# Kernel optimization log

Hardware: AMD Instinct MI355X
Metric: run time of the kernel (lower is better)

The kernel has to match this reference:

```python
import jax, jax.numpy as jnp
import numpy as np

N = 50000      # nodes per graph batch (per side)
E = 600000     # edges per side
B = 4096       # number of graphs (drug pairs)
D = 128        # node_dim == hidden_dim
K = 128        # kge_dim
R = 86         # rel_total
L = 3          # n_iter
EPS = 1e-5


def setup_inputs() -> dict:
    key = jax.random.key(0)
    ks = jax.random.split(key, 16)
    inp = {}
    inp["x1"] = jax.random.normal(ks[0], (N, D), jnp.float32)
    inp["x2"] = jax.random.normal(ks[1], (N, D), jnp.float32)
    inp["edge_index1"] = jax.random.randint(ks[2], (2, E), 0, N)
    inp["edge_index2"] = jax.random.randint(ks[3], (2, E), 0, N)
    inp["batch1"] = jnp.sort(jax.random.randint(ks[4], (N,), 0, B))
    inp["batch2"] = jnp.sort(jax.random.randint(ks[5], (N,), 0, B))
    inp["rel"] = jax.random.randint(ks[6], (B,), 0, R)
    # SAGEConv params, stacked over L layers (all [D,D] since node_dim==hidden_dim)
    sc = 0.05
    inp["Wl"] = jax.random.normal(ks[7], (L, D, D), jnp.float32) * sc   # lin on aggregated neighbors (has bias)
    inp["bl"] = jnp.zeros((L, D), jnp.float32)
    inp["Wr"] = jax.random.normal(ks[8], (L, D, D), jnp.float32) * sc   # root (self) lin, no bias
    # BatchNorm (eval mode: running stats)
    inp["bn_gamma"] = jnp.ones((L, D), jnp.float32)
    inp["bn_beta"] = jnp.zeros((L, D), jnp.float32)
    inp["bn_mean"] = jnp.zeros((L, D), jnp.float32)
    inp["bn_var"] = jnp.ones((L, D), jnp.float32)
    # relation embedding + final MLP
    inp["kge"] = jax.random.normal(ks[9], (R, K), jnp.float32)
    inp["W1"] = jax.random.normal(ks[10], (2 * D + K, D), jnp.float32) * sc
    inp["b1"] = jnp.zeros((D,), jnp.float32)
    inp["W2"] = jax.random.normal(ks[11], (D, 1), jnp.float32) * sc
    inp["b2"] = jnp.zeros((1,), jnp.float32)
    return inp


def _gnn(x, edge_index, Wl, bl, Wr, g, b, m, v):
    src, dst = edge_index[0], edge_index[1]
    deg = jax.ops.segment_sum(jnp.ones((E,), x.dtype), dst, num_segments=N)
    deg = jnp.maximum(deg, 1.0)[:, None]
    for i in range(L):
        agg = jax.ops.segment_sum(x[src], dst, num_segments=N) / deg  # mean aggregation
        h = agg @ Wl[i] + bl[i] + x @ Wr[i]                           # SAGEConv
        h = (h - m[i]) * (g[i] / jnp.sqrt(v[i] + EPS)) + b[i]         # BN (eval)
        x = jax.nn.relu(h)                                            # dropout = identity (eval)
    return x


def reference(x1, edge_index1, batch1, x2, edge_index2, batch2, rel,
              Wl, bl, Wr, bn_gamma, bn_beta, bn_mean, bn_var,
              kge, W1, b1, W2, b2):
    h1 = _gnn(x1, edge_index1, Wl, bl, Wr, bn_gamma, bn_beta, bn_mean, bn_var)
    h2 = _gnn(x2, edge_index2, Wl, bl, Wr, bn_gamma, bn_beta, bn_mean, bn_var)
    p1 = jax.ops.segment_sum(h1, batch1, num_segments=B)  # global_add_pool
    p2 = jax.ops.segment_sum(h2, batch2, num_segments=B)
    r = kge[rel]                                          # [B, K]
    z = jnp.concatenate([p1, p2, r], axis=-1)             # [B, 2D+K]
    h = jax.nn.relu(z @ W1 + b1)
    out = h @ W2 + b2
    return out.reshape(-1)
```

## Files before the change

kernel.cpp:

```cpp
#include <hip/hip_runtime.h>

#define NN 50000
#define NE 600000
#define NB 4096
#define DD 128
#define EPSV 1e-5f
#define NBKT 196
#define NCHUNK 256
#define CHSZ ((NE + NCHUNK - 1) / NCHUNK)

typedef __bf16 bf16x8 __attribute__((ext_vector_type(8)));
typedef float f32x4 __attribute__((ext_vector_type(4)));

__device__ inline unsigned short f2bf(float f) {
    unsigned u = __float_as_uint(f);
    u = (u + 0x7FFFu + ((u >> 16) & 1u)) >> 16;
    return (unsigned short)u;
}
__device__ inline float bf2f(unsigned short h) {
    return __uint_as_float(((unsigned)h) << 16);
}

__global__ void k_cvt(const float* __restrict__ x1, const float* __restrict__ x2,
                      unsigned short* __restrict__ xh, unsigned short* __restrict__ xl) {
    int i = blockIdx.x * 256 + threadIdx.x;
    if (i >= 2 * NN * 32) return;
    const float* x = (i < NN * 32) ? x1 : x2;
    int j = (i < NN * 32) ? i : i - NN * 32;
    float4 v = ((const float4*)x)[j];
    ushort4 h, l;
    h.x = f2bf(v.x); l.x = f2bf(v.x - bf2f(h.x));
    h.y = f2bf(v.y); l.y = f2bf(v.y - bf2f(h.y));
    h.z = f2bf(v.z); l.z = f2bf(v.z - bf2f(h.z));
    h.w = f2bf(v.w); l.w = f2bf(v.w - bf2f(h.w));
    ((ushort4*)xh)[i] = h;
    ((ushort4*)xl)[i] = l;
}

__global__ void k_wcvt(const float* __restrict__ W1, unsigned* __restrict__ wtp) {
    int t = blockIdx.x * 256 + threadIdx.x;
    if (t >= 128 * 384) return;
    int n = t / 384;
    int k = t - n * 384;
    float w = W1[k * 128 + n];
    unsigned short h = f2bf(w);
    unsigned short l = f2bf(w - bf2f(h));
    wtp[t] = ((unsigned)h << 16) | (unsigned)l;
}

__global__ void k_wfrag(const float* __restrict__ Wl, const float* __restrict__ Wr,
                        unsigned short* __restrict__ wf) {
    int t = blockIdx.x * 256 + threadIdx.x;
    if (t >= 3 * 128 * 256) return;
    int k = t & 255;
    int n = (t >> 8) & 127;
    int l = t >> 15;
    float w = (k < 128) ? Wl[l * 16384 + k * 128 + n] : Wr[l * 16384 + (k - 128) * 128 + n];
    unsigned short h = f2bf(w);
    unsigned short lo = f2bf(w - bf2f(h));
    int ntile = n >> 4, fm = n & 15, kc = k >> 5, kq = (k & 31) >> 3, j = k & 7;
    size_t pos = (size_t)l * 65536 + (size_t)(ntile * 8 + kc) * 1024 + (size_t)(kq * 16 + fm) * 8 + j;
    wf[pos] = h;
    wf[pos + 512] = lo;
}

__global__ void k_hist(const int* __restrict__ d0, const int* __restrict__ d1,
                       int* __restrict__ bcnt) {
    int side = (blockIdx.x >= NCHUNK) ? 1 : 0;
    int c = blockIdx.x - side * NCHUNK;
    const int* dst = side ? d1 : d0;
    int tid = threadIdx.x;
    __shared__ int h[NBKT];
    for (int i = tid; i < NBKT; i += 256) h[i] = 0;
    __syncthreads();
    int e0 = c * CHSZ, e1 = min(e0 + CHSZ, NE);
    for (int e = e0 + tid; e < e1; e += 256) atomicAdd(&h[dst[e] >> 8], 1);
    __syncthreads();
    int* bc = bcnt + ((size_t)side * NCHUNK + c) * NBKT;
    for (int i = tid; i < NBKT; i += 256) bc[i] = h[i];
}

__global__ void k_s1(int* __restrict__ bcnt, int* __restrict__ btot) {
    int side = (blockIdx.x >= NBKT) ? 1 : 0;
    int b = blockIdx.x - side * NBKT;
    int tid = threadIdx.x;
    int idx = ((size_t)side * NCHUNK + tid) * NBKT + b;
    int v = bcnt[idx];
    int lane = tid & 63, wv = tid >> 6;
    int x = v;
#pragma unroll
    for (int off = 1; off < 64; off <<= 1) {
        int y = __shfl_up(x, off, 64);
        if (lane >= off) x += y;
    }
    __shared__ int ws4[4];
    if (lane == 63) ws4[wv] = x;
    __syncthreads();
    int add = 0;
#pragma unroll
    for (int w = 0; w < 4; w++)
        if (w < wv) add += ws4[w];
    int incl = x + add;
    bcnt[idx] = incl - v;
    if (tid == 255) btot[side * NBKT + b] = incl;
}

__global__ void k_s2(const int* __restrict__ btot, int* __restrict__ bbase,
                     int* __restrict__ ptrC) {
    int side = blockIdx.x;
    int tid = threadIdx.x;
    int v = (tid < NBKT) ? btot[side * NBKT + tid] : 0;
    int lane = tid & 63, wv = tid >> 6;
    int x = v;
#pragma unroll
    for (int off = 1; off < 64; off <<= 1) {
        int y = __shfl_up(x, off, 64);
        if (lane >= off) x += y;
    }
    __shared__ int ws4[4];
    if (lane == 63) ws4[wv] = x;
    __syncthreads();
    int add = 0;
#pragma unroll
    for (int w = 0; w < 4; w++)
        if (w < wv) add += ws4[w];
    int incl = x + add;
    if (tid < NBKT) bbase[side * NBKT + tid] = incl - v;
    if (tid == 0 && side == 1) ptrC[2 * NN] = 2 * NE;
}

__global__ void k_part(const int* __restrict__ s0, const int* __restrict__ d0,
                       const int* __restrict__ s1, const int* __restrict__ d1,
                       const int* __restrict__ bcnt, const int* __restrict__ bbase,
                       int* __restrict__ part) {
    int side = (blockIdx.x >= NCHUNK) ? 1 : 0;
    int c = blockIdx.x - side * NCHUNK;
    const int* src = side ? s1 : s0;
    const int* dst = side ? d1 : d0;
    int tid = threadIdx.x;
    __shared__ int off[NBKT];
    const int* bc = bcnt + ((size_t)side * NCHUNK + c) * NBKT;
    for (int i = tid; i < NBKT; i += 256) off[i] = bbase[side * NBKT + i] + bc[i];
    __syncthreads();
    int e0 = c * CHSZ, e1 = min(e0 + CHSZ, NE);
    int* P = part + (size_t)side * NE;
    int soff = side * NN;
    for (int e = e0 + tid; e < e1; e += 256) {
        int d = dst[e];
        int pos = atomicAdd(&off[d >> 8], 1);
        P[pos] = ((src[e] + soff) << 8) | (d & 255);
    }
}

__global__ void k_csr(const int* __restrict__ part, const int* __restrict__ bbase,
                      int* __restrict__ ptrC, float* __restrict__ invdC,
                      int* __restrict__ csrC) {
    int side = (blockIdx.x >= NBKT) ? 1 : 0;
    int b = blockIdx.x - side * NBKT;
    int tid = threadIdx.x;
    const int* P = part + (size_t)side * NE;
    int base = bbase[side * NBKT + b];
    int endp = (b == NBKT - 1) ? NE : bbase[side * NBKT + b + 1];
    __shared__ int cnt[256];
    cnt[tid] = 0;
    __syncthreads();
    for (int e = base + tid; e < endp; e += 256) atomicAdd(&cnt[P[e] & 255], 1);
    __syncthreads();
    int v = cnt[tid];
    int lane = tid & 63, wv = tid >> 6;
    int x = v;
#pragma unroll
    for (int off = 1; off < 64; off <<= 1) {
        int y = __shfl_up(x, off, 64);
        if (lane >= off) x += y;
    }
    __shared__ int ws4[4];
    if (lane == 63) ws4[wv] = x;
    __syncthreads();
    int add = 0;
#pragma unroll
    for (int w = 0; w < 4; w++)
        if (w < wv) add += ws4[w];
    int excl = x + add - v;
    int node = (b << 8) + tid;
    if (node < NN) {
        ptrC[side * NN + node] = side * NE + base + excl;
        invdC[side * NN + node] = 1.0f / (float)(v > 1 ? v : 1);
    }
    __syncthreads();
    cnt[tid] = excl;
    __syncthreads();
    for (int e = base + tid; e < endp; e += 256) {
        int p = P[e];
        int pos = atomicAdd(&cnt[p & 255], 1);
        csrC[(size_t)side * NE + base + pos] = p >> 8;
    }
}

__global__ void k_gather(const unsigned short* __restrict__ xh, const int* __restrict__ ptr,
                         const int* __restrict__ csr, const float* __restrict__ invd,
                         unsigned short* __restrict__ aggH) {
    int wid = threadIdx.x >> 6;
    int lane = threadIdx.x & 63;
    int q = lane >> 4;
    int c = lane & 15;
    int n = blockIdx.x * 4 + wid;
    if (n >= 2 * NN) return;
    int beg = ptr[n], end = ptr[n + 1];
    float id = invd[n];
    float a[8];
#pragma unroll
    for (int k = 0; k < 8; k++) a[k] = 0.f;

    for (int base = beg; base < end; base += 64) {
        int cnt = min(end - base, 64);
        int idxv = csr[base + min(lane, cnt - 1)];
        for (int e0 = 0; e0 < cnt; e0 += 8) {
            int eA = e0 + q;
            int eB = e0 + 4 + q;
            int iA = __shfl(idxv, eA, 64);
            int iB = __shfl(idxv, eB, 64);
            float wA = (eA < cnt) ? 1.f : 0.f;
            float wB = (eB < cnt) ? 1.f : 0.f;
            uint4 vA = *(const uint4*)(xh + (((unsigned)iA << 7) + (c << 3)));
            uint4 vB = *(const uint4*)(xh + (((unsigned)iB << 7) + (c << 3)));
            a[0] += wA * __uint_as_float(vA.x << 16);
            a[1] += wA * __uint_as_float(vA.x & 0xffff0000u);
            a[2] += wA * __uint_as_float(vA.y << 16);
            a[3] += wA * __uint_as_float(vA.y & 0xffff0000u);
            a[4] += wA * __uint_as_float(vA.z << 16);
            a[5] += wA * __uint_as_float(vA.z & 0xffff0000u);
            a[6] += wA * __uint_as_float(vA.w << 16);
            a[7] += wA * __uint_as_float(vA.w & 0xffff0000u);
            a[0] += wB * __uint_as_float(vB.x << 16);
            a[1] += wB * __uint_as_float(vB.x & 0xffff0000u);
            a[2] += wB * __uint_as_float(vB.y << 16);
            a[3] += wB * __uint_as_float(vB.y & 0xffff0000u);
            a[4] += wB * __uint_as_float(vB.z << 16);
            a[5] += wB * __uint_as_float(vB.z & 0xffff0000u);
            a[6] += wB * __uint_as_float(vB.w << 16);
            a[7] += wB * __uint_as_float(vB.w & 0xffff0000u);
        }
    }
#pragma unroll
    for (int k = 0; k < 8; k++) {
        a[k] += __shfl_xor(a[k], 16, 64);
        a[k] += __shfl_xor(a[k], 32, 64);
    }
    if (q == 0) {
        unsigned short h0 = f2bf(a[0] * id), h1 = f2bf(a[1] * id);
        unsigned short h2 = f2bf(a[2] * id), h3 = f2bf(a[3] * id);
        unsigned short h4 = f2bf(a[4] * id), h5 = f2bf(a[5] * id);
        unsigned short h6 = f2bf(a[6] * id), h7 = f2bf(a[7] * id);
        uint4 o;
        o.x = (unsigned)h0 | ((unsigned)h1 << 16);
        o.y = (unsigned)h2 | ((unsigned)h3 << 16);
        o.z = (unsigned)h4 | ((unsigned)h5 << 16);
        o.w = (unsigned)h6 | ((unsigned)h7 << 16);
        *(uint4*)(aggH + (size_t)n * DD + c * 8) = o;
    }
}

__launch_bounds__(256)
__global__ void k_gemm2(const unsigned short* __restrict__ AH,
                        const unsigned short* __restrict__ XH, const unsigned short* __restrict__ XL,
                        const unsigned short* __restrict__ wf,
                        const float* __restrict__ bl, const float* __restrict__ g,
                        const float* __restrict__ be, const float* __restrict__ mn,
                        const float* __restrict__ vr,
                        unsigned short* __restrict__ OH, unsigned short* __restrict__ OL,
                        float* __restrict__ Of, int f32out) {
    int tid = threadIdx.x;
    int lane = tid & 63, w = tid >> 6;
    int fm = lane & 15, kq = lane >> 4;
    int m0 = blockIdx.x * 32;

    size_t rb0 = (size_t)(m0 + fm) * DD + kq * 8;
    size_t rb1 = rb0 + (size_t)16 * DD;
    const unsigned short* pA0 = AH + rb0;
    const unsigned short* pA1 = AH + rb1;
    const unsigned short* pXH0 = XH + rb0;
    const unsigned short* pXH1 = XH + rb1;
    const unsigned short* pXL0 = XL + rb0;
    const unsigned short* pXL1 = XL + rb1;
    const unsigned short* pW0 = wf + (size_t)(w * 2 + 0) * 8192 + lane * 8;
    const unsigned short* pW1 = wf + (size_t)(w * 2 + 1) * 8192 + lane * 8;

    f32x4 acc[2][2];
#pragma unroll
    for (int i = 0; i < 2; i++)
#pragma unroll
        for (int j = 0; j < 2; j++) acc[i][j] = (f32x4){0.f, 0.f, 0.f, 0.f};

#pragma unroll
    for (int c = 0; c < 8; c++) {
        bf16x8 a0h, a1h, a0l, a1l;
        if (c < 4) {
            a0h = *(const bf16x8*)(pA0 + c * 32);
            a1h = *(const bf16x8*)(pA1 + c * 32);
        } else {
            a0h = *(const bf16x8*)(pXH0 + (c - 4) * 32);
            a1h = *(const bf16x8*)(pXH1 + (c - 4) * 32);
            a0l = *(const bf16x8*)(pXL0 + (c - 4) * 32);
            a1l = *(const bf16x8*)(pXL1 + (c - 4) * 32);
        }
        bf16x8 w0h = *(const bf16x8*)(pW0 + c * 1024);
        bf16x8 w0l = *(const bf16x8*)(pW0 + c * 1024 + 512);
        bf16x8 w1h = *(const bf16x8*)(pW1 + c * 1024);
        bf16x8 w1l = *(const bf16x8*)(pW1 + c * 1024 + 512);
        acc[0][0] = __builtin_amdgcn_mfma_f32_16x16x32_bf16(a0h, w0h, acc[0][0], 0, 0, 0);
        acc[0][0] = __builtin_amdgcn_mfma_f32_16x16x32_bf16(a0h, w0l, acc[0][0], 0, 0, 0);
        acc[0][1] = __builtin_amdgcn_mfma_f32_16x16x32_bf16(a0h, w1h, acc[0][1], 0, 0, 0);
        acc[0][1] = __builtin_amdgcn_mfma_f32_16x16x32_bf16(a0h, w1l, acc[0][1], 0, 0, 0);
        acc[1][0] = __builtin_amdgcn_mfma_f32_16x16x32_bf16(a1h, w0h, acc[1][0], 0, 0, 0);
        acc[1][0] = __builtin_amdgcn_mfma_f32_16x16x32_bf16(a1h, w0l, acc[1][0], 0, 0, 0);
        acc[1][1] = __builtin_amdgcn_mfma_f32_16x16x32_bf16(a1h, w1h, acc[1][1], 0, 0, 0);
        acc[1][1] = __builtin_amdgcn_mfma_f32_16x16x32_bf16(a1h, w1l, acc[1][1], 0, 0, 0);
        if (c >= 4) {
            acc[0][0] = __builtin_amdgcn_mfma_f32_16x16x32_bf16(a0l, w0h, acc[0][0], 0, 0, 0);
            acc[0][1] = __builtin_amdgcn_mfma_f32_16x16x32_bf16(a0l, w1h, acc[0][1], 0, 0, 0);
            acc[1][0] = __builtin_amdgcn_mfma_f32_16x16x32_bf16(a1l, w0h, acc[1][0], 0, 0, 0);
            acc[1][1] = __builtin_amdgcn_mfma_f32_16x16x32_bf16(a1l, w1h, acc[1][1], 0, 0, 0);
        }
    }

    float scv[2], shv[2];
#pragma unroll
    for (int nt = 0; nt < 2; nt++) {
        int jj = w * 32 + nt * 16 + fm;
        float s = g[jj] * rsqrtf(vr[jj] + EPSV);
        scv[nt] = s;
        shv[nt] = (bl[jj] - mn[jj]) * s + be[jj];
    }
#pragma unroll
    for (int mt = 0; mt < 2; mt++) {
#pragma unroll
        for (int r = 0; r < 4; r++) {
            int grow = m0 + mt * 16 + kq * 4 + r;
#pragma unroll
            for (int nt = 0; nt < 2; nt++) {
                int gcol = w * 32 + nt * 16 + fm;
                float o = fmaxf(acc[mt][nt][r] * scv[nt] + shv[nt], 0.f);
                if (f32out) {
                    Of[(size_t)grow * DD + gcol] = o;
                } else {
                    unsigned short h = f2bf(o);
                    OH[(size_t)grow * DD + gcol] = h;
                    OL[(size_t)grow * DD + gcol] = f2bf(o - bf2f(h));
                }
            }
        }
    }
}

__launch_bounds__(128)
__global__ void k_pool2(const float* __restrict__ cf, const int* __restrict__ bt1,
                        const int* __restrict__ bt2, float* __restrict__ ppool) {
    int side = (blockIdx.x >= NB) ? 1 : 0;
    int b = blockIdx.x - side * NB;
    const int* batch = side ? bt2 : bt1;
    const float* h = cf + (size_t)side * NN * DD;
    __shared__ int sr[2];
    if (threadIdx.x < 2) {
        int target = b + (int)threadIdx.x;
        int lo = 0, hi = NN;
        while (lo < hi) {
            int mid = (lo + hi) >> 1;
            if (batch[mid] < target) lo = mid + 1; else hi = mid;
        }
        sr[threadIdx.x] = lo;
    }
    __syncthreads();
    int beg = sr[0], end = sr[1];
    int t = threadIdx.x;
    float acc = 0.f;
    for (int r = beg; r < end; r++) acc += h[(size_t)r * DD + t];
    ppool[((size_t)side * NB + b) * DD + t] = acc;
}

__global__ void k_zb(const float* __restrict__ ppool, const int* __restrict__ rel,
                     const float* __restrict__ kge,
                     unsigned short* __restrict__ zh, unsigned short* __restrict__ zl) {
    int t = blockIdx.x * 256 + threadIdx.x;
    if (t >= NB * 384) return;
    int b = t / 384;
    int j = t - b * 384;
    float v;
    if (j < 128) v = ppool[(size_t)b * DD + j];
    else if (j < 256) v = ppool[(size_t)NB * DD + (size_t)b * DD + (j - 128)];
    else v = kge[(size_t)rel[b] * 128 + (j - 256)];
    unsigned short h = f2bf(v);
    zh[t] = h;
    zl[t] = f2bf(v - bf2f(h));
}

__launch_bounds__(256)
__global__ void k_mlp2(const unsigned short* __restrict__ zh, const unsigned short* __restrict__ zl,
                       const unsigned* __restrict__ w1p,
                       const float* __restrict__ b1, const float* __restrict__ W2,
                       const float* __restrict__ b2, float* __restrict__ out) {
    __shared__ __align__(16) unsigned short sZ[2][32 * 40];
    __shared__ __align__(16) unsigned short sW[2][128 * 40];
    __shared__ float hpart[32][4];
    int tid = threadIdx.x;
    int m0 = blockIdx.x * 32;
    int lane = tid & 63, w = tid >> 6;
    int fm = lane & 15, q = lane >> 4;
    int wn = w * 32;

    f32x4 acc[2][2];
#pragma unroll
    for (int i = 0; i < 2; i++)
#pragma unroll
        for (int j = 0; j < 2; j++) acc[i][j] = (f32x4){0.f, 0.f, 0.f, 0.f};

    for (int c = 0; c < 12; c++) {
        int k0 = c * 32;
        __syncthreads();
        {
            int row = tid >> 3, seg = tid & 7;
            size_t off = (size_t)(m0 + row) * 384 + k0 + seg * 4;
            *(ushort4*)&sZ[0][row * 40 + seg * 4] = *(const ushort4*)(zh + off);
            *(ushort4*)&sZ[1][row * 40 + seg * 4] = *(const ushort4*)(zl + off);
        }
#pragma unroll
        for (int i = 0; i < 4; i++) {
            int u = tid + 256 * i;
            int row = u >> 3, seg = u & 7;
            uint4 val = *(const uint4*)(w1p + (size_t)row * 384 + k0 + seg * 4);
            ushort4 hi, lo;
            hi.x = val.x >> 16; hi.y = val.y >> 16; hi.z = val.z >> 16; hi.w = val.w >> 16;
            lo.x = val.x & 0xFFFF; lo.y = val.y & 0xFFFF; lo.z = val.z & 0xFFFF; lo.w = val.w & 0xFFFF;
            *(ushort4*)&sW[0][row * 40 + seg * 4] = hi;
            *(ushort4*)&sW[1][row * 40 + seg * 4] = lo;
        }
        __syncthreads();
        bf16x8 zfh[2], zfl[2];
#pragma unroll
        for (int mt = 0; mt < 2; mt++) {
            int r = mt * 16 + fm;
            zfh[mt] = *(const bf16x8*)&sZ[0][r * 40 + q * 8];
            zfl[mt] = *(const bf16x8*)&sZ[1][r * 40 + q * 8];
        }
#pragma unroll
        for (int nt = 0; nt < 2; nt++) {
            int nr = wn + nt * 16 + fm;
            bf16x8 wh = *(const bf16x8*)&sW[0][nr * 40 + q * 8];
            bf16x8 wl = *(const bf16x8*)&sW[1][nr * 40 + q * 8];
#pragma unroll
            for (int mt = 0; mt < 2; mt++) {
                acc[mt][nt] = __builtin_amdgcn_mfma_f32_16x16x32_bf16(zfh[mt], wh, acc[mt][nt], 0, 0, 0);
                acc[mt][nt] = __builtin_amdgcn_mfma_f32_16x16x32_bf16(zfh[mt], wl, acc[mt][nt], 0, 0, 0);
                acc[mt][nt] = __builtin_amdgcn_mfma_f32_16x16x32_bf16(zfl[mt], wh, acc[mt][nt], 0, 0, 0);
            }
        }
    }

    float b1v[2], w2v[2];
#pragma unroll
    for (int nt = 0; nt < 2; nt++) {
        int col = wn + nt * 16 + fm;
        b1v[nt] = b1[col];
        w2v[nt] = W2[col];
    }
#pragma unroll
    for (int mt = 0; mt < 2; mt++) {
#pragma unroll
        for (int r = 0; r < 4; r++) {
            float val = 0.f;
#pragma unroll
            for (int nt = 0; nt < 2; nt++)
                val += fmaxf(acc[mt][nt][r] + b1v[nt], 0.f) * w2v[nt];
#pragma unroll
            for (int m = 1; m < 16; m <<= 1) val += __shfl_xor(val, m, 64);
            if (fm == 0) hpart[mt * 16 + q * 4 + r][w] = val;
        }
    }
    __syncthreads();
    if (tid < 32)
        out[m0 + tid] = hpart[tid][0] + hpart[tid][1] + hpart[tid][2] + hpart[tid][3] + b2[0];
}

extern "C" void kernel_launch(void* const* d_in, const int* in_sizes, int n_in,
                              void* d_out, int out_size, void* d_ws, size_t ws_size,
                              hipStream_t stream) {
    const float* x1  = (const float*)d_in[0];
    const float* x2  = (const float*)d_in[1];
    const int*   ei1 = (const int*)d_in[2];
    const int*   ei2 = (const int*)d_in[3];
    const int*   bt1 = (const int*)d_in[4];
    const int*   bt2 = (const int*)d_in[5];
    const int*   rel = (const int*)d_in[6];
    const float* Wl  = (const float*)d_in[7];
    const float* bl  = (const float*)d_in[8];
    const float* Wr  = (const float*)d_in[9];
    const float* g   = (const float*)d_in[10];
    const float* be  = (const float*)d_in[11];
    const float* mn  = (const float*)d_in[12];
    const float* vr  = (const float*)d_in[13];
    const float* kge = (const float*)d_in[14];
    const float* W1  = (const float*)d_in[15];
    const float* b1v = (const float*)d_in[16];
    const float* W2  = (const float*)d_in[17];
    const float* b2v = (const float*)d_in[18];

    char* ws = (char*)d_ws;
    size_t off = 0;
    auto alloc = [&](size_t bytes) {
        void* p = ws + off;
        off += (bytes + 255) & ~(size_t)255;
        return p;
    };
    const size_t PL = (size_t)2 * NN * DD;
    unsigned short* xbufH = (unsigned short*)alloc(PL * 2);
    unsigned short* xbufL = (unsigned short*)alloc(PL * 2);
    unsigned short* obufH = (unsigned short*)alloc(PL * 2);
    unsigned short* obufL = (unsigned short*)alloc(PL * 2);
    unsigned short* aggH  = (unsigned short*)alloc(PL * 2);
    unsigned short* wf = (unsigned short*)alloc((size_t)3 * 65536 * 2);
    unsigned* wtp  = (unsigned*)alloc((size_t)128 * 384 * 4);
    float* ppool   = (float*)alloc((size_t)2 * NB * DD * 4);
    unsigned short* zh = (unsigned short*)alloc((size_t)NB * 384 * 2);
    unsigned short* zl = (unsigned short*)alloc((size_t)NB * 384 * 2);
    int*   bcnt    = (int*)alloc((size_t)2 * NCHUNK * NBKT * 4);
    int*   btot    = (int*)alloc((size_t)2 * NBKT * 4);
    int*   bbase   = (int*)alloc((size_t)2 * NBKT * 4);
    int*   part    = (int*)alloc((size_t)2 * NE * 4);
    int*   ptrC    = (int*)alloc((size_t)(2 * NN + 1) * 4);
    float* invdC   = (float*)alloc((size_t)2 * NN * 4);
    int*   csrC    = (int*)alloc((size_t)2 * NE * 4);
    if (off > ws_size) return;

    float* cf = (float*)obufH;

    const int nbCvt   = 12500;
    const int nbNode4 = (2 * NN + 3) / 4;
    const int nbGemm2 = 2 * NN / 32;
    const int nbW     = (128 * 384 + 255) / 256;
    const int nbWf    = (3 * 128 * 256 + 255) / 256;

    k_wcvt<<<nbW, 256, 0, stream>>>(W1, wtp);
    k_wfrag<<<nbWf, 256, 0, stream>>>(Wl, Wr, wf);

    k_hist<<<2 * NCHUNK, 256, 0, stream>>>(ei1 + NE, ei2 + NE, bcnt);
    k_s1<<<2 * NBKT, 256, 0, stream>>>(bcnt, btot);
    k_s2<<<2, 256, 0, stream>>>(btot, bbase, ptrC);
    k_part<<<2 * NCHUNK, 256, 0, stream>>>(ei1, ei1 + NE, ei2, ei2 + NE, bcnt, bbase, part);
    k_csr<<<2 * NBKT, 256, 0, stream>>>(part, bbase, ptrC, invdC, csrC);

    k_cvt<<<nbCvt, 256, 0, stream>>>(x1, x2, xbufH, xbufL);

    k_gather<<<nbNode4, 256, 0, stream>>>(xbufH, ptrC, csrC, invdC, aggH);
    k_gemm2<<<nbGemm2, 256, 0, stream>>>(aggH, xbufH, xbufL, wf, bl, g, be, mn, vr,
                                         obufH, obufL, (float*)nullptr, 0);
    k_gather<<<nbNode4, 256, 0, stream>>>(obufH, ptrC, csrC, invdC, aggH);
    k_gemm2<<<nbGemm2, 256, 0, stream>>>(aggH, obufH, obufL, wf + 65536, bl + 128, g + 128,
                                         be + 128, mn + 128, vr + 128,
                                         xbufH, xbufL, (float*)nullptr, 0);
    k_gather<<<nbNode4, 256, 0, stream>>>(xbufH, ptrC, csrC, invdC, aggH);
    k_gemm2<<<nbGemm2, 256, 0, stream>>>(aggH, xbufH, xbufL, wf + 131072, bl + 256, g + 256,
                                         be + 256, mn + 256, vr + 256,
                                         (unsigned short*)nullptr, (unsigned short*)nullptr, cf, 1);

    k_pool2<<<2 * NB, 128, 0, stream>>>(cf, bt1, bt2, ppool);
    k_zb<<<(NB * 384 + 255) / 256, 256, 0, stream>>>(ppool, rel, kge, zh, zl);
    k_mlp2<<<NB / 32, 256, 0, stream>>>(zh, zl, wtp, b1v, W2, b2v, (float*)d_out);
}
```

Measured before the change: 501.5 us.

## Stage per-column-group GEMM weights in LDS and reassign waves to row tiles

The SAGE GEMM kernel is restructured so each block handles one 32-column output group across 128 rows. The block's weight fragment (32 KB) is staged into shared memory once, and each wave reads it from LDS instead of reloading weights from global memory. Each wave then covers its own 32 rows, which reduces per-wave weight traffic. In exchange the kernel adds an LDS copy and a barrier, reads the activation rows four times across column groups, and sets an occupancy hint of five blocks per CU.

```diff
diff --git a/kernel.cpp b/kernel.cpp
--- a/kernel.cpp
+++ b/kernel.cpp
@@ -261,8 +261,8 @@
     }
 }
 
-__launch_bounds__(256)
-__global__ void k_gemm2(const unsigned short* __restrict__ AH,
+__launch_bounds__(256, 5)
+__global__ void k_gemm3(const unsigned short* __restrict__ AH,
                         const unsigned short* __restrict__ XH, const unsigned short* __restrict__ XL,
                         const unsigned short* __restrict__ wf,
                         const float* __restrict__ bl, const float* __restrict__ g,
@@ -270,12 +270,26 @@
                         const float* __restrict__ vr,
                         unsigned short* __restrict__ OH, unsigned short* __restrict__ OL,
                         float* __restrict__ Of, int f32out) {
+    __shared__ __align__(16) unsigned short sW[16384];
     int tid = threadIdx.x;
     int lane = tid & 63, w = tid >> 6;
     int fm = lane & 15, kq = lane >> 4;
-    int m0 = blockIdx.x * 32;
-
-    size_t rb0 = (size_t)(m0 + fm) * DD + kq * 8;
+    int gx = blockIdx.x;
+    int grp = gx & 3;
+    int m0 = (gx >> 2) * 128;
+
+    {
+        const uint4* src = (const uint4*)wf + (size_t)grp * 2048;
+        uint4* dst = (uint4*)sW;
+#pragma unroll
+        for (int i = 0; i < 8; i++) dst[tid + 256 * i] = src[tid + 256 * i];
+    }
+    __syncthreads();
+
+    int rbase = m0 + w * 32;
+    if (rbase >= 2 * NN) return;
+
+    size_t rb0 = (size_t)(rbase + fm) * DD + kq * 8;
     size_t rb1 = rb0 + (size_t)16 * DD;
     const unsigned short* pA0 = AH + rb0;
     const unsigned short* pA1 = AH + rb1;
@@ -283,8 +297,7 @@
     const unsigned short* pXH1 = XH + rb1;
     const unsigned short* pXL0 = XL + rb0;
     const unsigned short* pXL1 = XL + rb1;
-    const unsigned short* pW0 = wf + (size_t)(w * 2 + 0) * 8192 + lane * 8;
-    const unsigned short* pW1 = wf + (size_t)(w * 2 + 1) * 8192 + lane * 8;
+    const unsigned short* pWl = sW + lane * 8;
 
     f32x4 acc[2][2];
 #pragma unroll
@@ -304,10 +317,10 @@
             a0l = *(const bf16x8*)(pXL0 + (c - 4) * 32);
             a1l = *(const bf16x8*)(pXL1 + (c - 4) * 32);
         }
-        bf16x8 w0h = *(const bf16x8*)(pW0 + c * 1024);
-        bf16x8 w0l = *(const bf16x8*)(pW0 + c * 1024 + 512);
-        bf16x8 w1h = *(const bf16x8*)(pW1 + c * 1024);
-        bf16x8 w1l = *(const bf16x8*)(pW1 + c * 1024 + 512);
+        bf16x8 w0h = *(const bf16x8*)(pWl + c * 1024);
+        bf16x8 w0l = *(const bf16x8*)(pWl + c * 1024 + 512);
+        bf16x8 w1h = *(const bf16x8*)(pWl + (8 + c) * 1024);
+        bf16x8 w1l = *(const bf16x8*)(pWl + (8 + c) * 1024 + 512);
         acc[0][0] = __builtin_amdgcn_mfma_f32_16x16x32_bf16(a0h, w0h, acc[0][0], 0, 0, 0);
         acc[0][0] = __builtin_amdgcn_mfma_f32_16x16x32_bf16(a0h, w0l, acc[0][0], 0, 0, 0);
         acc[0][1] = __builtin_amdgcn_mfma_f32_16x16x32_bf16(a0h, w1h, acc[0][1], 0, 0, 0);
@@ -327,7 +340,7 @@
     float scv[2], shv[2];
 #pragma unroll
     for (int nt = 0; nt < 2; nt++) {
-        int jj = w * 32 + nt * 16 + fm;
+        int jj = grp * 32 + nt * 16 + fm;
         float s = g[jj] * rsqrtf(vr[jj] + EPSV);
         scv[nt] = s;
         shv[nt] = (bl[jj] - mn[jj]) * s + be[jj];
@@ -336,10 +349,10 @@
     for (int mt = 0; mt < 2; mt++) {
 #pragma unroll
         for (int r = 0; r < 4; r++) {
-            int grow = m0 + mt * 16 + kq * 4 + r;
+            int grow = rbase + mt * 16 + kq * 4 + r;
 #pragma unroll
             for (int nt = 0; nt < 2; nt++) {
-                int gcol = w * 32 + nt * 16 + fm;
+                int gcol = grp * 32 + nt * 16 + fm;
                 float o = fmaxf(acc[mt][nt][r] * scv[nt] + shv[nt], 0.f);
                 if (f32out) {
                     Of[(size_t)grow * DD + gcol] = o;
@@ -535,7 +548,7 @@
 
     const int nbCvt   = 12500;
     const int nbNode4 = (2 * NN + 3) / 4;
-    const int nbGemm2 = 2 * NN / 32;
+    const int nbGemm3 = ((2 * NN + 127) / 128) * 4;
     const int nbW     = (128 * 384 + 255) / 256;
     const int nbWf    = (3 * 128 * 256 + 255) / 256;
 
@@ -551,14 +564,14 @@
     k_cvt<<<nbCvt, 256, 0, stream>>>(x1, x2, xbufH, xbufL);
 
     k_gather<<<nbNode4, 256, 0, stream>>>(xbufH, ptrC, csrC, invdC, aggH);
-    k_gemm2<<<nbGemm2, 256, 0, stream>>>(aggH, xbufH, xbufL, wf, bl, g, be, mn, vr,
+    k_gemm3<<<nbGemm3, 256, 0, stream>>>(aggH, xbufH, xbufL, wf, bl, g, be, mn, vr,
                                          obufH, obufL, (float*)nullptr, 0);
     k_gather<<<nbNode4, 256, 0, stream>>>(obufH, ptrC, csrC, invdC, aggH);
-    k_gemm2<<<nbGemm2, 256, 0, stream>>>(aggH, obufH, obufL, wf + 65536, bl + 128, g + 128,
+    k_gemm3<<<nbGemm3, 256, 0, stream>>>(aggH, obufH, obufL, wf + 65536, bl + 128, g + 128,
                                          be + 128, mn + 128, vr + 128,
                                          xbufH, xbufL, (float*)nullptr, 0);
     k_gather<<<nbNode4, 256, 0, stream>>>(xbufH, ptrC, csrC, invdC, aggH);
-    k_gemm2<<<nbGemm2, 256, 0, stream>>>(aggH, xbufH, xbufL, wf + 131072, bl + 256, g + 256,
+    k_gemm3<<<nbGemm3, 256, 0, stream>>>(aggH, xbufH, xbufL, wf + 131072, bl + 256, g + 256,
                                          be + 256, mn + 256, vr + 256,
                                          (unsigned short*)nullptr, (unsigned short*)nullptr, cf, 1);
 
```

Result: no change. 508.0 us (+1.3%).
